# Optimization experiments

Hardware: AMD Instinct MI355X
Metric: run time of the kernel (lower is better)

The kernel has to match this reference:

```python
import jax, jax.numpy as jnp
import numpy as np


def cmul(a, b):
    # complex multiply on (..., 2) real/imag pairs
    ar, ai = a[..., 0], a[..., 1]
    br, bi = b[..., 0], b[..., 1]
    return jnp.stack([ar * br - ai * bi, ar * bi + ai * br], axis=-1)


def butterfly_apply(x, diag, subdiag, superdiag, k):
    # x: [B, n, 2]; tridiagonal-at-offset-k complex matrix applied to x.
    # diag: [n, 2]; subdiag/superdiag padded to [n, 2], first n-k entries used.
    n = x.shape[-2]
    out = cmul(diag, x)
    out = out.at[..., k:, :].add(cmul(subdiag[: n - k], x[..., : n - k, :]))
    out = out.at[..., : n - k, :].add(cmul(superdiag[: n - k], x[..., k:, :]))
    return out


def block_perm(x, logit, s):
    # Soft block permutation: within each contiguous block of size s,
    # mix identity with even-odd separation (prob p0), then mix each half
    # with its reversal (probs p1, p2). Acts identically on real & imag.
    B, n, _ = x.shape
    p = jax.nn.sigmoid(logit)
    y = x.reshape(B, n // s, s, 2)
    eo = jnp.concatenate([y[:, :, 0::2, :], y[:, :, 1::2, :]], axis=2)
    y = (1 - p[0]) * y + p[0] * eo
    h = s // 2
    first = (1 - p[1]) * y[:, :, :h, :] + p[1] * jnp.flip(y[:, :, :h, :], axis=2)
    second = (1 - p[2]) * y[:, :, h:, :] + p[2] * jnp.flip(y[:, :, h:, :], axis=2)
    return jnp.concatenate([first, second], axis=2).reshape(B, n, 2)


def trifat_forward(x, perm_logits, diags, subdiags, superdiags, bias):
    B, n = x.shape
    depth, m = diags.shape[0], diags.shape[1]
    perm_sizes = [n >> i for i in range(m - 1)][::-1]  # 4, 8, ..., n
    # real_to_complex: zero imaginary part
    xc = jnp.stack([x, jnp.zeros_like(x)], axis=-1)  # [B, n, 2]
    for d in range(depth):
        for j, s in enumerate(perm_sizes):
            xc = block_perm(xc, perm_logits[d, j], s)
        for i in range(m):
            k = n >> (i + 1)  # offsets n/2, n/4, ..., 1
            xc = butterfly_apply(xc, diags[d, i], subdiags[d, i], superdiags[d, i], k)
    return xc[..., 0] + bias  # take real part, add bias


def setup_inputs() -> dict:
    key = jax.random.key(0)
    ks = jax.random.split(key, 6)
    B, n, depth = 4096, 1024, 2
    m = int(np.log2(n))
    return {
        "x": jax.random.normal(ks[0], (B, n), jnp.float32),
        "perm_logits": jax.random.normal(ks[1], (depth, m - 1, 3), jnp.float32),
        "diags": jax.random.normal(ks[2], (depth, m, n, 2), jnp.float32),
        "subdiags": jax.random.normal(ks[3], (depth, m, n, 2), jnp.float32),
        "superdiags": jax.random.normal(ks[4], (depth, m, n, 2), jnp.float32),
        "bias": jnp.zeros((n,), jnp.float32),
    }


def reference(x, perm_logits, diags, subdiags, superdiags, bias):
    return trifat_forward(x, perm_logits, diags, subdiags, superdiags, bias)
```

## Files before the change

kernel.cpp:

```cpp
#include <hip/hip_runtime.h>

#define N 1024
#define THREADS 256
#define EPT 4

__device__ __forceinline__ float2* run_pipeline(
    float2* bufA, float2* bufB, int tid,
    const float* __restrict__ logits,
    const float* __restrict__ diags,
    const float* __restrict__ subd,
    const float* __restrict__ supd)
{
    float2* src = bufA;
    float2* dst = bufB;

    for (int d = 0; d < 2; ++d) {
        for (int j = 0; j < 9; ++j) {
            const int s = 4 << j;
            const int h = s >> 1;
            const float* lg = logits + (d * 9 + j) * 3;
            const float p0 = 1.0f / (1.0f + expf(-lg[0]));
            const float p1 = 1.0f / (1.0f + expf(-lg[1]));
            const float p2 = 1.0f / (1.0f + expf(-lg[2]));
#pragma unroll
            for (int e = 0; e < EPT; ++e) {
                const int idx = tid + e * THREADS;
                const int base = idx & ~(s - 1);
                const int t = idx & (s - 1);
                const bool lo = (t < h);

                const int eo_t = lo ? (2 * t) : (2 * (t - h) + 1);
                const float2 xt  = src[idx];
                const float2 xeo = src[base + eo_t];
                float2 yt;
                yt.x = xt.x + p0 * (xeo.x - xt.x);
                yt.y = xt.y + p0 * (xeo.y - xt.y);

                const int tm = lo ? (h - 1 - t) : (s + h - 1 - t);
                const float psel = lo ? p1 : p2;
                const int eo_m = (tm < h) ? (2 * tm) : (2 * (tm - h) + 1);
                const float2 xm   = src[base + tm];
                const float2 xmeo = src[base + eo_m];
                float2 ym;
                ym.x = xm.x + p0 * (xmeo.x - xm.x);
                ym.y = xm.y + p0 * (xmeo.y - xm.y);

                float2 o;
                o.x = yt.x + psel * (ym.x - yt.x);
                o.y = yt.y + psel * (ym.y - yt.y);
                dst[idx] = o;
            }
            __syncthreads();
            float2* tmp = src; src = dst; dst = tmp;
        }
        for (int i = 0; i < 10; ++i) {
            const int k = N >> (i + 1);
            const float2* Dg = (const float2*)(diags + (size_t)((d * 10 + i) * N) * 2);
            const float2* Sb = (const float2*)(subd  + (size_t)((d * 10 + i) * N) * 2);
            const float2* Sp = (const float2*)(supd  + (size_t)((d * 10 + i) * N) * 2);
#pragma unroll
            for (int e = 0; e < EPT; ++e) {
                const int idx = tid + e * THREADS;
                const float2 xv = src[idx];
                const float2 dg = Dg[idx];
                float2 o;
                o.x = dg.x * xv.x - dg.y * xv.y;
                o.y = dg.x * xv.y + dg.y * xv.x;
                if (idx >= k) {
                    const float2 xs = src[idx - k];
                    const float2 sb = Sb[idx - k];
                    o.x += sb.x * xs.x - sb.y * xs.y;
                    o.y += sb.x * xs.y + sb.y * xs.x;
                }
                if (idx < N - k) {
                    const float2 xp = src[idx + k];
                    const float2 sp = Sp[idx];
                    o.x += sp.x * xp.x - sp.y * xp.y;
                    o.y += sp.x * xp.y + sp.y * xp.x;
                }
                dst[idx] = o;
            }
            __syncthreads();
            float2* tmp = src; src = dst; dst = tmp;
        }
    }
    return src;
}

__global__ __launch_bounds__(THREADS) void trifat_kernel(
    const float* __restrict__ x,
    const float* __restrict__ logits,
    const float* __restrict__ diags,
    const float* __restrict__ subd,
    const float* __restrict__ supd,
    const float* __restrict__ bias,
    float* __restrict__ out,
    int B)
{
    __shared__ float2 bufA[N];
    __shared__ float2 bufB[N];

    const int row = blockIdx.x;
    const int tid = threadIdx.x;
    if (row >= B) return;

    const float* xr = x + (size_t)row * N;
#pragma unroll
    for (int e = 0; e < EPT; ++e) {
        int idx = tid + e * THREADS;
        bufA[idx] = make_float2(xr[idx], 0.0f);
    }
    __syncthreads();

    float2* res = run_pipeline(bufA, bufB, tid, logits, diags, subd, supd);

    float* orow = out + (size_t)row * N;
#pragma unroll
    for (int e = 0; e < EPT; ++e) {
        int idx = tid + e * THREADS;
        orow[idx] = res[idx].x + bias[idx];
    }
}

#define TBW 512

__global__ __launch_bounds__(TBW) void build_W(
    const float* __restrict__ logits,
    const float* __restrict__ diags,
    const float* __restrict__ subd,
    const float* __restrict__ supd,
    float* __restrict__ W)
{
    __shared__ float2 buf[2][2][N];

    const int j0 = blockIdx.x * 2;
    const int tid = threadIdx.x;

#pragma unroll
    for (int v = 0; v < 2; ++v)
#pragma unroll
        for (int e = 0; e < 2; ++e) {
            const int idx = tid + e * TBW;
            buf[0][v][idx] = make_float2(idx == (j0 + v) ? 1.0f : 0.0f, 0.0f);
        }
    __syncthreads();

    int sb = 0;
    for (int d = 0; d < 2; ++d) {
        for (int jp = 0; jp < 9; ++jp) {
            const int s = 4 << jp;
            const int h = s >> 1;
            const int hh = s >> 2;
            const float* lg = logits + (d * 9 + jp) * 3;
            const float p0 = 1.0f / (1.0f + expf(-lg[0]));
            const float p1 = 1.0f / (1.0f + expf(-lg[1]));
            const float p2 = 1.0f / (1.0f + expf(-lg[2]));
#pragma unroll
            for (int e = 0; e < 2; ++e) {
                const int tau = tid + e * TBW;
                const int v = tau >> 9;
                const int pid = tau & 511;
                const int w = pid & ((s >> 1) - 1);
                const int base = (pid >> (jp + 1)) << (jp + 2);

                int t, tm;
                float psel;
                if (w < hh) { t = w;          tm = h - 1 - w;  psel = p1; }
                else        { const int u = w - hh; t = h + u; tm = s - 1 - u; psel = p2; }

                const int eot = (t  < h) ? (2 * t)  : (2 * (t  - h) + 1);
                const int eom = (tm < h) ? (2 * tm) : (2 * (tm - h) + 1);

                const float2* src = buf[sb][v];
                float2* dst = buf[sb ^ 1][v];

                const float2 xt = src[base + t],  xet = src[base + eot];
                const float2 xm = src[base + tm], xem = src[base + eom];
                float2 yt, ym;
                yt.x = xt.x + p0 * (xet.x - xt.x);
                yt.y = xt.y + p0 * (xet.y - xt.y);
                ym.x = xm.x + p0 * (xem.x - xm.x);
                ym.y = xm.y + p0 * (xem.y - xm.y);

                float2 ot, om;
                ot.x = yt.x + psel * (ym.x - yt.x);
                ot.y = yt.y + psel * (ym.y - yt.y);
                om.x = ym.x + psel * (yt.x - ym.x);
                om.y = ym.y + psel * (yt.y - ym.y);
                dst[base + t]  = ot;
                dst[base + tm] = om;
            }
            __syncthreads();
            sb ^= 1;
        }
        for (int i = 0; i < 10; ++i) {
            const int k = N >> (i + 1);
            const float2* Dg  = (const float2*)(diags + (size_t)((d * 10 + i) * N) * 2);
            const float2* Sbc = (const float2*)(subd  + (size_t)((d * 10 + i) * N) * 2);
            const float2* Spc = (const float2*)(supd  + (size_t)((d * 10 + i) * N) * 2);
#pragma unroll
            for (int e = 0; e < 2; ++e) {
                const int idx = tid + e * TBW;
                const float2 dg = Dg[idx];
                float2 sbv = make_float2(0.f, 0.f), spv = make_float2(0.f, 0.f);
                if (idx >= k)     sbv = Sbc[idx - k];
                if (idx < N - k)  spv = Spc[idx];
#pragma unroll
                for (int v = 0; v < 2; ++v) {
                    const float2* src = buf[sb][v];
                    const float2 xv = src[idx];
                    float2 o;
                    o.x = dg.x * xv.x - dg.y * xv.y;
                    o.y = dg.x * xv.y + dg.y * xv.x;
                    if (idx >= k) {
                        const float2 xs = src[idx - k];
                        o.x += sbv.x * xs.x - sbv.y * xs.y;
                        o.y += sbv.x * xs.y + sbv.y * xs.x;
                    }
                    if (idx < N - k) {
                        const float2 xp = src[idx + k];
                        o.x += spv.x * xp.x - spv.y * xp.y;
                        o.y += spv.x * xp.y + spv.y * xp.x;
                    }
                    buf[sb ^ 1][v][idx] = o;
                }
            }
            __syncthreads();
            sb ^= 1;
        }
    }

#pragma unroll
    for (int v = 0; v < 2; ++v)
#pragma unroll
        for (int e = 0; e < 2; ++e) {
            const int idx = tid + e * TBW;
            W[(size_t)(j0 + v) * N + idx] = buf[sb][v][idx].x;
        }
}

__device__ __forceinline__ unsigned short f2bf_rne(float f) {
    unsigned int u = __float_as_uint(f);
    unsigned int r = u + 0x7fffu + ((u >> 16) & 1u);
    return (unsigned short)(r >> 16);
}

__global__ __launch_bounds__(THREADS) void transpose_split(
    const float* __restrict__ W, unsigned short* __restrict__ Bt)
{
    __shared__ float tile[64][65];
    const int j0 = blockIdx.x * 64;
    const int n0 = blockIdx.y * 64;
    const int t = threadIdx.x;
    const int c = t & 63;
    const int rb = t >> 6;

#pragma unroll
    for (int rr = 0; rr < 16; ++rr) {
        const int r = rr * 4 + rb;
        tile[r][c] = W[(size_t)(j0 + r) * N + n0 + c];
    }
    __syncthreads();
#pragma unroll
    for (int rr = 0; rr < 16; ++rr) {
        const int r = rr * 4 + rb;
        const float v = tile[c][r];
        Bt[(size_t)(n0 + r) * N + j0 + c] = f2bf_rne(v);
    }
}

__global__ __launch_bounds__(THREADS) void conv_x(
    const float* __restrict__ x, unsigned short* __restrict__ A2)
{
    const int gid = blockIdx.x * THREADS + threadIdx.x;
    const float4 v = *(const float4*)(x + (size_t)gid * 4);
    ushort4 o;
    o.x = f2bf_rne(v.x);
    o.y = f2bf_rne(v.y);
    o.z = f2bf_rne(v.z);
    o.w = f2bf_rne(v.w);
    *(ushort4*)(A2 + (size_t)gid * 4) = o;
}

typedef __attribute__((ext_vector_type(8))) __bf16 bf16x8;
typedef __attribute__((ext_vector_type(4))) float f32x4;

#define GLB(p) ((const __attribute__((address_space(1))) void*)(p))
#define LDS(p) ((__attribute__((address_space(3))) void*)(p))

__global__ __launch_bounds__(THREADS) void gemm_bf16(
    const unsigned short* __restrict__ A2,
    const unsigned short* __restrict__ Bt,
    const float* __restrict__ bias,
    float* __restrict__ out)
{
    __shared__ __align__(16) unsigned short As[2][128 * 64];
    __shared__ __align__(16) unsigned short Bs[2][128 * 64];

    const int m0 = blockIdx.x * 128;
    const int n0 = blockIdx.y * 128;
    const int tid = threadIdx.x;
    const int wave = tid >> 6, lane = tid & 63;
    const int wm = (wave >> 1) * 64, wn = (wave & 1) * 64;
    const int lrow = lane & 15, q = lane >> 4;
    const int r7 = lrow & 7;

    f32x4 acc[4][4] = {};

    auto issue = [&](int kt, int bsel) {
        const int k0 = kt * 64;
        const unsigned short* gA = A2 + (size_t)m0 * N + k0;
        const unsigned short* gB = Bt + (size_t)n0 * N + k0;
#pragma unroll
        for (int r = 0; r < 4; ++r) {
            const int s = r * 256 + tid;
            const int row = s >> 3;
            const int gl = (s & 7) ^ (row & 7);
            __builtin_amdgcn_global_load_lds(GLB(gA + (size_t)row * N + gl * 8),
                                             LDS(&As[bsel][s * 8]), 16, 0, 0);
            __builtin_amdgcn_global_load_lds(GLB(gB + (size_t)row * N + gl * 8),
                                             LDS(&Bs[bsel][s * 8]), 16, 0, 0);
        }
    };

    issue(0, 0);
    __syncthreads();

    for (int kt = 0; kt < 16; ++kt) {
        const int cur = kt & 1;
        if (kt + 1 < 16) issue(kt + 1, cur ^ 1);

#pragma unroll
        for (int kk = 0; kk < 64; kk += 32) {
            const int pg = ((kk >> 3) + q) ^ r7;
            bf16x8 a[4], b[4];
#pragma unroll
            for (int mi = 0; mi < 4; ++mi)
                a[mi] = *(const bf16x8*)(&As[cur][(wm + mi * 16 + lrow) * 64 + pg * 8]);
#pragma unroll
            for (int ni = 0; ni < 4; ++ni)
                b[ni] = *(const bf16x8*)(&Bs[cur][(wn + ni * 16 + lrow) * 64 + pg * 8]);
#pragma unroll
            for (int mi = 0; mi < 4; ++mi)
#pragma unroll
                for (int ni = 0; ni < 4; ++ni)
                    acc[mi][ni] = __builtin_amdgcn_mfma_f32_16x16x32_bf16(
                        a[mi], b[ni], acc[mi][ni], 0, 0, 0);
        }
        __syncthreads();
    }

#pragma unroll
    for (int ni = 0; ni < 4; ++ni) {
        const int col = n0 + wn + ni * 16 + lrow;
        const float bv = bias[col];
#pragma unroll
        for (int mi = 0; mi < 4; ++mi)
#pragma unroll
            for (int r = 0; r < 4; ++r) {
                const int row = m0 + wm + mi * 16 + q * 4 + r;
                out[(size_t)row * N + col] = acc[mi][ni][r] + bv;
            }
    }
}

extern "C" void kernel_launch(void* const* d_in, const int* in_sizes, int n_in,
                              void* d_out, int out_size, void* d_ws, size_t ws_size,
                              hipStream_t stream) {
    const float* x      = (const float*)d_in[0];
    const float* logits = (const float*)d_in[1];
    const float* diags  = (const float*)d_in[2];
    const float* subd   = (const float*)d_in[3];
    const float* supd   = (const float*)d_in[4];
    const float* bias   = (const float*)d_in[5];
    float* out = (float*)d_out;

    const int B = in_sizes[0] / N;

    const size_t off_W  = 0;
    const size_t off_Bt = 4u * 1024 * 1024;
    const size_t off_A2 = off_Bt + 2u * 1024 * 1024;
    const size_t need   = off_A2 + (size_t)B * N * 2;

    if (ws_size >= need && (B % 128) == 0) {
        float* W           = (float*)((char*)d_ws + off_W);
        unsigned short* Bt = (unsigned short*)((char*)d_ws + off_Bt);
        unsigned short* A2 = (unsigned short*)((char*)d_ws + off_A2);

        conv_x<<<dim3(B * N / (THREADS * 4)), dim3(THREADS), 0, stream>>>(x, A2);
        build_W<<<dim3(N / 2), dim3(TBW), 0, stream>>>(logits, diags, subd, supd, W);
        transpose_split<<<dim3(16, 16), dim3(THREADS), 0, stream>>>(W, Bt);
        gemm_bf16<<<dim3(B / 128, 8), dim3(THREADS), 0, stream>>>(A2, Bt, bias, out);
    } else {
        trifat_kernel<<<dim3(B), dim3(THREADS), 0, stream>>>(
            x, logits, diags, subd, supd, bias, out, B);
    }
}
```

Measured before the change: 145.8 us.

## Fuse x conversion, W build and transpose into one prep kernel

Merges the bf16 conversion of x, the W construction and the transpose/bf16 split into a single launch. Extra blocks handle the x conversion while the other blocks build columns of W and write them directly as transposed bf16 into Bt. This drops the fp32 W buffer and the separate transpose pass, and saves two launches. The direct transposed store is strided by N per element, so writes are uncoalesced. The fast path is now restricted to B == 4096.

Measured after the change: 140.5 us. 3.6% less time.

```diff
diff --git a/kernel.cpp b/kernel.cpp
--- a/kernel.cpp
+++ b/kernel.cpp
@@ -122,19 +122,46 @@
     }
 }
 
+__device__ __forceinline__ unsigned short f2bf_rne(float f) {
+    unsigned int u = __float_as_uint(f);
+    unsigned int r = u + 0x7fffu + ((u >> 16) & 1u);
+    return (unsigned short)(r >> 16);
+}
+
 #define TBW 512
-
-__global__ __launch_bounds__(TBW) void build_W(
+#define NB_BUILD 512
+
+__global__ __launch_bounds__(TBW) void prep_kernel(
     const float* __restrict__ logits,
     const float* __restrict__ diags,
     const float* __restrict__ subd,
     const float* __restrict__ supd,
-    float* __restrict__ W)
+    const float* __restrict__ x,
+    unsigned short* __restrict__ Bt,
+    unsigned short* __restrict__ A2)
 {
     __shared__ float2 buf[2][2][N];
 
+    const int tid = threadIdx.x;
+
+    if (blockIdx.x >= NB_BUILD) {
+        const int cb = blockIdx.x - NB_BUILD;
+        const size_t base4 = (size_t)cb * 4096;
+#pragma unroll
+        for (int r = 0; r < 8; ++r) {
+            const size_t g4 = base4 + r * 512 + tid;
+            const float4 v = *(const float4*)(x + g4 * 4);
+            ushort4 o;
+            o.x = f2bf_rne(v.x);
+            o.y = f2bf_rne(v.y);
+            o.z = f2bf_rne(v.z);
+            o.w = f2bf_rne(v.w);
+            *(ushort4*)(A2 + g4 * 4) = o;
+        }
+        return;
+    }
+
     const int j0 = blockIdx.x * 2;
-    const int tid = threadIdx.x;
 
 #pragma unroll
     for (int v = 0; v < 2; ++v)
@@ -235,51 +262,8 @@
 #pragma unroll
         for (int e = 0; e < 2; ++e) {
             const int idx = tid + e * TBW;
-            W[(size_t)(j0 + v) * N + idx] = buf[sb][v][idx].x;
-        }
-}
-
-__device__ __forceinline__ unsigned short f2bf_rne(float f) {
-    unsigned int u = __float_as_uint(f);
-    unsigned int r = u + 0x7fffu + ((u >> 16) & 1u);
-    return (unsigned short)(r >> 16);
-}
-
-__global__ __launch_bounds__(THREADS) void transpose_split(
-    const float* __restrict__ W, unsigned short* __restrict__ Bt)
-{
-    __shared__ float tile[64][65];
-    const int j0 = blockIdx.x * 64;
-    const int n0 = blockIdx.y * 64;
-    const int t = threadIdx.x;
-    const int c = t & 63;
-    const int rb = t >> 6;
-
-#pragma unroll
-    for (int rr = 0; rr < 16; ++rr) {
-        const int r = rr * 4 + rb;
-        tile[r][c] = W[(size_t)(j0 + r) * N + n0 + c];
-    }
-    __syncthreads();
-#pragma unroll
-    for (int rr = 0; rr < 16; ++rr) {
-        const int r = rr * 4 + rb;
-        const float v = tile[c][r];
-        Bt[(size_t)(n0 + r) * N + j0 + c] = f2bf_rne(v);
-    }
-}
-
-__global__ __launch_bounds__(THREADS) void conv_x(
-    const float* __restrict__ x, unsigned short* __restrict__ A2)
-{
-    const int gid = blockIdx.x * THREADS + threadIdx.x;
-    const float4 v = *(const float4*)(x + (size_t)gid * 4);
-    ushort4 o;
-    o.x = f2bf_rne(v.x);
-    o.y = f2bf_rne(v.y);
-    o.z = f2bf_rne(v.z);
-    o.w = f2bf_rne(v.w);
-    *(ushort4*)(A2 + (size_t)gid * 4) = o;
+            Bt[(size_t)idx * N + (j0 + v)] = f2bf_rne(buf[sb][v][idx].x);
+        }
 }
 
 typedef __attribute__((ext_vector_type(8))) __bf16 bf16x8;
@@ -377,19 +361,16 @@
 
     const int B = in_sizes[0] / N;
 
-    const size_t off_W  = 0;
-    const size_t off_Bt = 4u * 1024 * 1024;
-    const size_t off_A2 = off_Bt + 2u * 1024 * 1024;
+    const size_t off_Bt = 0;
+    const size_t off_A2 = 2u * 1024 * 1024;
     const size_t need   = off_A2 + (size_t)B * N * 2;
 
-    if (ws_size >= need && (B % 128) == 0) {
-        float* W           = (float*)((char*)d_ws + off_W);
+    if (ws_size >= need && B == 4096) {
         unsigned short* Bt = (unsigned short*)((char*)d_ws + off_Bt);
         unsigned short* A2 = (unsigned short*)((char*)d_ws + off_A2);
 
-        conv_x<<<dim3(B * N / (THREADS * 4)), dim3(THREADS), 0, stream>>>(x, A2);
-        build_W<<<dim3(N / 2), dim3(TBW), 0, stream>>>(logits, diags, subd, supd, W);
-        transpose_split<<<dim3(16, 16), dim3(THREADS), 0, stream>>>(W, Bt);
+        prep_kernel<<<dim3(NB_BUILD + 256), dim3(TBW), 0, stream>>>(
+            logits, diags, subd, supd, x, Bt, A2);
         gemm_bf16<<<dim3(B / 128, 8), dim3(THREADS), 0, stream>>>(A2, Bt, bias, out);
     } else {
         trifat_kernel<<<dim3(B), dim3(THREADS), 0, stream>>>(
```
